# Performance work log

Measured on AMD Instinct MI355X. Metric: run time of the kernel, lower is better.

Reference implementation:

```python
import jax, jax.numpy as jnp
import numpy as np

B, L, H, V = 32768, 24, 64, 64
EPS_NORM = 1e-12  # F.normalize eps
EPS_LN = 1e-5     # LayerNorm eps


def setup_inputs() -> dict:
    key = jax.random.key(0)
    ks = jax.random.split(key, 12)
    s = 1.0 / np.sqrt(H)
    init_val = float(np.log(0.9184 / (1.0 - 0.9184)))
    return {
        "seq": jax.random.randint(ks[0], (B, L), 0, V, dtype=jnp.int32),
        "embed": jax.random.normal(ks[1], (V, H), jnp.float32),
        "w1": jax.random.normal(ks[2], (H, 2 * H), jnp.float32) * s,
        "b1": jnp.zeros((2 * H,), jnp.float32),
        "w2": jax.random.normal(ks[3], (2 * H, H), jnp.float32) * s,
        "b2": jnp.zeros((H,), jnp.float32),
        "ln_g": jnp.ones((H,), jnp.float32),
        "ln_b": jnp.zeros((H,), jnp.float32),
        "rp_w": jax.random.normal(ks[4], (H, H), jnp.float32) * s,
        "rp_b": jnp.zeros((H,), jnp.float32),
        "out_w": jax.random.normal(ks[5], (H, V), jnp.float32) * s,
        "out_b": jnp.zeros((V,), jnp.float32),
        "alpha_logits": jnp.full((L,), init_val, jnp.float32),
    }


def _layernorm(x, g, b):
    mu = jnp.mean(x, axis=-1, keepdims=True)
    var = jnp.mean(jnp.square(x - mu), axis=-1, keepdims=True)
    return (x - mu) * jax.lax.rsqrt(var + EPS_LN) * g + b


def reference(seq, embed, w1, b1, w2, b2, ln_g, ln_b, rp_w, rp_b, out_w, out_b, alpha_logits):
    h = embed[seq]  # [B, L, H]
    ff = jax.nn.relu(h @ w1 + b1) @ w2 + b2
    h = _layernorm(h + ff, ln_g, ln_b)

    alphas = jax.nn.sigmoid(alpha_logits) * 0.49 + 0.5  # [L]
    ht = jnp.swapaxes(h[:, :-1, :], 0, 1)  # [L-1, B, H] time-major

    def step(M, inp):
        k, a = inp  # k: [B, H], a: scalar
        kn = k / jnp.maximum(jnp.linalg.norm(k, axis=-1, keepdims=True), EPS_NORM)
        vp = jnp.einsum('bij,bj->bi', M, kn)
        dv = k - vp
        M = M + (1.0 - a) * (dv[:, :, None] * kn[:, None, :])
        return M, None

    M0 = jnp.zeros((seq.shape[0], h.shape[-1], h.shape[-1]), h.dtype)
    M, _ = jax.lax.scan(step, M0, (ht, alphas[:-1]))

    v = jnp.einsum('bij,bj->bi', M, h[:, -1, :])
    return (v @ rp_w + rp_b) @ out_w + out_b  # [B, V]
```

## Files before the change

### kernel.cpp

```cpp
#include <hip/hip_runtime.h>
#include <hip/hip_bf16.h>
#include <math.h>

#define B_SZ 32768
#define L_SZ 24
#define H_SZ 64
#define V_SZ 64

#define KN_WS 0
#define WK_WS 4096
#define NRM_WS 8192
#define B2_WS 8256
#define CF_WS 8320
#define G_WS  8384
#define WS_F  12480

#define ROW 96
#define G_L   0
#define WK_L  4096
#define NRM_L 10240
#define CB_L  10304
#define TO_L  11840
#define LDS_F 13376

__global__ __launch_bounds__(64) void k_tab(
    const float* __restrict__ embed, const float* __restrict__ w1, const float* __restrict__ b1,
    const float* __restrict__ w2, const float* __restrict__ b2,
    const float* __restrict__ ln_g, const float* __restrict__ ln_b,
    const float* __restrict__ rp_w, const float* __restrict__ rp_b,
    const float* __restrict__ out_w, const float* __restrict__ out_b,
    const float* __restrict__ alpha_logits, float* __restrict__ ws)
{
  const int v = blockIdx.x;
  const int j = threadIdx.x;

  if (v < V_SZ) {
    const float ev = embed[v * H_SZ + j];
    float h0 = b1[j], h1 = b1[j + 64];
    #pragma unroll
    for (int k = 0; k < H_SZ; ++k) {
      const float ek = __shfl(ev, k);
      h0 = fmaf(ek, w1[k * 128 + j], h0);
      h1 = fmaf(ek, w1[k * 128 + 64 + j], h1);
    }
    h0 = fmaxf(h0, 0.0f);
    h1 = fmaxf(h1, 0.0f);
    float x = ev + b2[j];
    #pragma unroll
    for (int k = 0; k < H_SZ; ++k) {
      x = fmaf(__shfl(h0, k), w2[k * H_SZ + j], x);
      x = fmaf(__shfl(h1, k), w2[(k + 64) * H_SZ + j], x);
    }
    float mu = x;
    #pragma unroll
    for (int m = 1; m < 64; m <<= 1) mu += __shfl_xor(mu, m);
    mu *= (1.0f / 64.0f);
    const float dv = x - mu;
    float var = dv * dv;
    #pragma unroll
    for (int m = 1; m < 64; m <<= 1) var += __shfl_xor(var, m);
    var *= (1.0f / 64.0f);
    const float y = dv * rsqrtf(var + 1e-5f) * ln_g[j] + ln_b[j];
    float n2 = y * y;
    #pragma unroll
    for (int m = 1; m < 64; m <<= 1) n2 += __shfl_xor(n2, m);
    const float nrm = sqrtf(n2);
    const float rn = 1.0f / fmaxf(nrm, 1e-12f);
    ws[KN_WS + v * H_SZ + j] = y * rn;
    if (j == 0) ws[NRM_WS + v] = nrm;
    float t1 = 0.0f;
    #pragma unroll
    for (int k = 0; k < H_SZ; ++k) t1 = fmaf(__shfl(y, k), rp_w[k * H_SZ + j], t1);
    float wk = 0.0f;
    #pragma unroll
    for (int k = 0; k < H_SZ; ++k) wk = fmaf(__shfl(t1, k), out_w[k * V_SZ + j], wk);
    ws[WK_WS + v * H_SZ + j] = wk;
  } else {
    float s = out_b[j];
    #pragma unroll
    for (int k = 0; k < H_SZ; ++k) s = fmaf(rp_b[k], out_w[k * V_SZ + j], s);
    ws[B2_WS + j] = s;
    if (j < L_SZ) {
      float cf = 0.0f;
      if (j < L_SZ - 1) {
        const float a = 1.0f / (1.0f + expf(-alpha_logits[j])) * 0.49f + 0.5f;
        cf = 1.0f - a;
      }
      ws[CF_WS + j] = cf;
    }
  }
}

__global__ __launch_bounds__(64) void k_gram(float* __restrict__ ws)
{
  const int u = blockIdx.x;
  const int j = threadIdx.x;
  const float a = ws[KN_WS + u * H_SZ + j];
  float r[64];
  const float4* rp = (const float4*)(ws + KN_WS + j * H_SZ);
  #pragma unroll
  for (int i = 0; i < 16; ++i) {
    const float4 f = rp[i];
    r[4 * i] = f.x; r[4 * i + 1] = f.y; r[4 * i + 2] = f.z; r[4 * i + 3] = f.w;
  }
  float s = 0.0f;
  #pragma unroll
  for (int k = 0; k < 64; ++k) s = fmaf(__shfl(a, k), r[k], s);
  ws[G_WS + u * H_SZ + j] = s;
}

__global__ __launch_bounds__(256) void k_scan(
    const int* __restrict__ seq, const float* __restrict__ ws, float* __restrict__ out)
{
  __shared__ float lds[LDS_F];
  const int tid = threadIdx.x;
  const float4* ws4 = (const float4*)ws;

  for (int i = tid; i < 1024; i += 256)
    ((float4*)(lds + G_L))[i] = ws4[G_WS / 4 + i];
  for (int i = tid; i < 1024; i += 256) {
    const float4 f = ws4[WK_WS / 4 + i];
    const int r = i >> 4;
    const int c = (i & 15) * 4;
    *(float4*)(lds + WK_L + r * ROW + 12 * (c >> 3) + (c & 7)) = f;
  }
  if (tid < 16) ((float4*)(lds + NRM_L))[tid] = ws4[NRM_WS / 4 + tid];
  __syncthreads();

  const int lane = tid & 63;
  const int wv = tid >> 6;
  const float* cfg = ws + CF_WS;

  if (lane < 16) {
    const int ab = wv * 16 + lane;
    const int batch = blockIdx.x * 64 + ab;
    int g[24];
    const int4* sp = (const int4*)(seq + batch * L_SZ);
    #pragma unroll
    for (int i = 0; i < 6; ++i) {
      const int4 t4 = sp[i];
      g[4 * i] = t4.x; g[4 * i + 1] = t4.y; g[4 * i + 2] = t4.z; g[4 * i + 3] = t4.w;
    }
    int* tob = (int*)lds + TO_L + ab * 24;
    #pragma unroll
    for (int i = 0; i < 6; ++i)
      ((int4*)tob)[i] = make_int4(g[4 * i] * ROW, g[4 * i + 1] * ROW,
                                  g[4 * i + 2] * ROW, g[4 * i + 3] * ROW);
    const int q = g[23];
    const float nl = lds[NRM_L + q];
    const float* Gt = lds + G_L;
    float* cb = lds + CB_L + ab * 24;
    float P[23];
    #pragma unroll
    for (int t = 0; t < 23; ++t) P[t] = 0.0f;
    #pragma unroll
    for (int s = 22; s >= 0; --s) {
      const float base = nl * Gt[(g[s] << 6) + q];
      const float cs = cfg[s] * (base - P[s]);
      cb[s] = cs;
      #pragma unroll
      for (int t = 0; t < s; ++t)
        P[t] = fmaf(cs, Gt[(g[t] << 6) + g[s]], P[t]);
    }
    cb[23] = 0.0f;
  }
  __syncthreads();

  const int grp = lane >> 3;
  const int s8 = lane & 7;
  const int cbse = 12 * s8;
  const float* wkL = lds + WK_L;
  const float* b2g = ws + B2_WS + s8 * 8;
  const float4 bA = *(const float4*)(b2g);
  const float4 bB = *(const float4*)(b2g + 4);

  #pragma unroll
  for (int it = 0; it < 2; ++it) {
    const int ab = wv * 16 + it * 8 + grp;
    const int batch = blockIdx.x * 64 + ab;
    float cv[24]; int tv[24];
    const float4* cp = (const float4*)(lds + CB_L + ab * 24);
    const int4* tp = (const int4*)((const int*)lds + TO_L + ab * 24);
    #pragma unroll
    for (int i = 0; i < 6; ++i) {
      const float4 f = cp[i];
      cv[4 * i] = f.x; cv[4 * i + 1] = f.y; cv[4 * i + 2] = f.z; cv[4 * i + 3] = f.w;
      const int4 t4 = tp[i];
      tv[4 * i] = t4.x; tv[4 * i + 1] = t4.y; tv[4 * i + 2] = t4.z; tv[4 * i + 3] = t4.w;
    }
    float oa[8] = {bA.x, bA.y, bA.z, bA.w, bB.x, bB.y, bB.z, bB.w};
    #pragma unroll
    for (int t = 0; t < 23; ++t) {
      const float c = cv[t];
      const float* wr = wkL + tv[t] + cbse;
      const float4 wa = *(const float4*)wr;
      const float4 wb = *(const float4*)(wr + 4);
      oa[0] = fmaf(c, wa.x, oa[0]); oa[1] = fmaf(c, wa.y, oa[1]);
      oa[2] = fmaf(c, wa.z, oa[2]); oa[3] = fmaf(c, wa.w, oa[3]);
      oa[4] = fmaf(c, wb.x, oa[4]); oa[5] = fmaf(c, wb.y, oa[5]);
      oa[6] = fmaf(c, wb.z, oa[6]); oa[7] = fmaf(c, wb.w, oa[7]);
    }
    float4* op = (float4*)(out + batch * V_SZ + s8 * 8);
    op[0] = make_float4(oa[0], oa[1], oa[2], oa[3]);
    op[1] = make_float4(oa[4], oa[5], oa[6], oa[7]);
  }
}

extern "C" void kernel_launch(void* const* d_in, const int* in_sizes, int n_in,
                              void* d_out, int out_size, void* d_ws, size_t ws_size,
                              hipStream_t stream)
{
  const int*   seq          = (const int*)d_in[0];
  const float* embed        = (const float*)d_in[1];
  const float* w1           = (const float*)d_in[2];
  const float* b1           = (const float*)d_in[3];
  const float* w2           = (const float*)d_in[4];
  const float* b2           = (const float*)d_in[5];
  const float* ln_g         = (const float*)d_in[6];
  const float* ln_b         = (const float*)d_in[7];
  const float* rp_w         = (const float*)d_in[8];
  const float* rp_b         = (const float*)d_in[9];
  const float* out_w        = (const float*)d_in[10];
  const float* out_b        = (const float*)d_in[11];
  const float* alpha_logits = (const float*)d_in[12];
  float* ws   = (float*)d_ws;
  float* outp = (float*)d_out;

  hipLaunchKernelGGL(k_tab, dim3(V_SZ + 1), dim3(64), 0, stream,
                     embed, w1, b1, w2, b2, ln_g, ln_b,
                     rp_w, rp_b, out_w, out_b, alpha_logits, ws);
  hipLaunchKernelGGL(k_gram, dim3(V_SZ), dim3(64), 0, stream, ws);
  hipLaunchKernelGGL(k_scan, dim3(B_SZ / 64), dim3(256), 0, stream,
                     seq, ws, outp);
}
```

Before: 27.84 us.

## Shrink scan blocks to one wave so every lane runs a batch recurrence

The scan kernel now uses 64-thread blocks instead of 256-thread blocks. All 64 lanes compute the backward coefficient recurrence, one batch each, where before only 16 lanes per wave did. Token indices are packed four per int in LDS. The norm, bias and coefficient tail is staged in LDS instead of read from global memory. The trade-off is fewer waves per CU: table staging and the output accumulation (now 8 iterations per wave) run on a single wave with less latency hiding.

```diff
diff --git a/kernel.cpp b/kernel.cpp
--- a/kernel.cpp
+++ b/kernel.cpp
@@ -16,12 +16,12 @@
 #define WS_F  12480
 
 #define ROW 96
-#define G_L   0
-#define WK_L  4096
-#define NRM_L 10240
-#define CB_L  10304
-#define TO_L  11840
-#define LDS_F 13376
+#define G_L    0
+#define WK_L   4096
+#define C_L    10240
+#define TK_L   12032
+#define TAIL_L 12544
+#define LDS_F  12704
 
 __global__ __launch_bounds__(64) void k_tab(
     const float* __restrict__ embed, const float* __restrict__ w1, const float* __restrict__ b1,
@@ -109,31 +109,32 @@
   ws[G_WS + u * H_SZ + j] = s;
 }
 
-__global__ __launch_bounds__(256) void k_scan(
+__global__ __launch_bounds__(64) void k_scan(
     const int* __restrict__ seq, const float* __restrict__ ws, float* __restrict__ out)
 {
   __shared__ float lds[LDS_F];
-  const int tid = threadIdx.x;
+  const int lane = threadIdx.x;
   const float4* ws4 = (const float4*)ws;
 
-  for (int i = tid; i < 1024; i += 256)
-    ((float4*)(lds + G_L))[i] = ws4[G_WS / 4 + i];
-  for (int i = tid; i < 1024; i += 256) {
+  float4* g4 = (float4*)(lds + G_L);
+  for (int i = lane; i < 1024; i += 64) g4[i] = ws4[G_WS / 4 + i];
+  for (int i = lane; i < 1024; i += 64) {
     const float4 f = ws4[WK_WS / 4 + i];
     const int r = i >> 4;
-    const int c = (i & 15) * 4;
-    *(float4*)(lds + WK_L + r * ROW + 12 * (c >> 3) + (c & 7)) = f;
-  }
-  if (tid < 16) ((float4*)(lds + NRM_L))[tid] = ws4[NRM_WS / 4 + tid];
+    const int c4 = (i & 15) * 4;
+    *(float4*)(lds + WK_L + r * ROW + 12 * (c4 >> 3) + (c4 & 4)) = f;
+  }
+  if (lane < 38) ((float4*)(lds + TAIL_L))[lane] = ws4[NRM_WS / 4 + lane];
   __syncthreads();
 
-  const int lane = tid & 63;
-  const int wv = tid >> 6;
-  const float* cfg = ws + CF_WS;
-
-  if (lane < 16) {
-    const int ab = wv * 16 + lane;
-    const int batch = blockIdx.x * 64 + ab;
+  const float* nrmL = lds + TAIL_L;
+  const float* b2L  = lds + TAIL_L + 64;
+  const float* cfL  = lds + TAIL_L + 128;
+  const float* Gt   = lds + G_L;
+
+  const int batch0 = blockIdx.x * 64;
+  {
+    const int batch = batch0 + lane;
     int g[24];
     const int4* sp = (const int4*)(seq + batch * L_SZ);
     #pragma unroll
@@ -141,58 +142,71 @@
       const int4 t4 = sp[i];
       g[4 * i] = t4.x; g[4 * i + 1] = t4.y; g[4 * i + 2] = t4.z; g[4 * i + 3] = t4.w;
     }
-    int* tob = (int*)lds + TO_L + ab * 24;
+    int tw[8];
     #pragma unroll
     for (int i = 0; i < 6; ++i)
-      ((int4*)tob)[i] = make_int4(g[4 * i] * ROW, g[4 * i + 1] * ROW,
-                                  g[4 * i + 2] * ROW, g[4 * i + 3] * ROW);
+      tw[i] = g[4 * i] | (g[4 * i + 1] << 8) | (g[4 * i + 2] << 16) | (g[4 * i + 3] << 24);
+    tw[6] = 0; tw[7] = 0;
+    int* tkb = (int*)lds + TK_L + lane * 8;
+    ((int4*)tkb)[0] = make_int4(tw[0], tw[1], tw[2], tw[3]);
+    ((int4*)tkb)[1] = make_int4(tw[4], tw[5], tw[6], tw[7]);
+
+    float cfv[24];
+    #pragma unroll
+    for (int i = 0; i < 6; ++i) {
+      const float4 f = ((const float4*)cfL)[i];
+      cfv[4 * i] = f.x; cfv[4 * i + 1] = f.y; cfv[4 * i + 2] = f.z; cfv[4 * i + 3] = f.w;
+    }
+
     const int q = g[23];
-    const float nl = lds[NRM_L + q];
-    const float* Gt = lds + G_L;
-    float* cb = lds + CB_L + ab * 24;
-    float P[23];
+    const float nl = nrmL[q];
+    float P[23], carr[24];
     #pragma unroll
     for (int t = 0; t < 23; ++t) P[t] = 0.0f;
     #pragma unroll
     for (int s = 22; s >= 0; --s) {
       const float base = nl * Gt[(g[s] << 6) + q];
-      const float cs = cfg[s] * (base - P[s]);
-      cb[s] = cs;
+      const float cs = cfv[s] * (base - P[s]);
+      carr[s] = cs;
       #pragma unroll
       for (int t = 0; t < s; ++t)
         P[t] = fmaf(cs, Gt[(g[t] << 6) + g[s]], P[t]);
     }
-    cb[23] = 0.0f;
+    carr[23] = 0.0f;
+    float* cb = lds + C_L + lane * 28;
+    #pragma unroll
+    for (int i = 0; i < 6; ++i)
+      ((float4*)cb)[i] = make_float4(carr[4 * i], carr[4 * i + 1], carr[4 * i + 2], carr[4 * i + 3]);
   }
   __syncthreads();
 
   const int grp = lane >> 3;
   const int s8 = lane & 7;
-  const int cbse = 12 * s8;
+  const int cb12 = 12 * s8;
+  const float4 bA = ((const float4*)(b2L + s8 * 8))[0];
+  const float4 bB = ((const float4*)(b2L + s8 * 8))[1];
   const float* wkL = lds + WK_L;
-  const float* b2g = ws + B2_WS + s8 * 8;
-  const float4 bA = *(const float4*)(b2g);
-  const float4 bB = *(const float4*)(b2g + 4);
 
   #pragma unroll
-  for (int it = 0; it < 2; ++it) {
-    const int ab = wv * 16 + it * 8 + grp;
-    const int batch = blockIdx.x * 64 + ab;
-    float cv[24]; int tv[24];
-    const float4* cp = (const float4*)(lds + CB_L + ab * 24);
-    const int4* tp = (const int4*)((const int*)lds + TO_L + ab * 24);
+  for (int it = 0; it < 8; ++it) {
+    const int ab = it * 8 + grp;
+    float cv[24];
+    const float4* cp = (const float4*)(lds + C_L + ab * 28);
     #pragma unroll
     for (int i = 0; i < 6; ++i) {
       const float4 f = cp[i];
       cv[4 * i] = f.x; cv[4 * i + 1] = f.y; cv[4 * i + 2] = f.z; cv[4 * i + 3] = f.w;
-      const int4 t4 = tp[i];
-      tv[4 * i] = t4.x; tv[4 * i + 1] = t4.y; tv[4 * i + 2] = t4.z; tv[4 * i + 3] = t4.w;
-    }
+    }
+    const int4* tp = (const int4*)((const int*)lds + TK_L + ab * 8);
+    const int4 ta = tp[0], tb = tp[1];
+    int tw[6] = {ta.x, ta.y, ta.z, ta.w, tb.x, tb.y};
+
     float oa[8] = {bA.x, bA.y, bA.z, bA.w, bB.x, bB.y, bB.z, bB.w};
     #pragma unroll
     for (int t = 0; t < 23; ++t) {
       const float c = cv[t];
-      const float* wr = wkL + tv[t] + cbse;
+      const int tok = (tw[t >> 2] >> ((t & 3) * 8)) & 63;
+      const float* wr = wkL + tok * ROW + cb12;
       const float4 wa = *(const float4*)wr;
       const float4 wb = *(const float4*)(wr + 4);
       oa[0] = fmaf(c, wa.x, oa[0]); oa[1] = fmaf(c, wa.y, oa[1]);
@@ -200,7 +214,7 @@
       oa[4] = fmaf(c, wb.x, oa[4]); oa[5] = fmaf(c, wb.y, oa[5]);
       oa[6] = fmaf(c, wb.z, oa[6]); oa[7] = fmaf(c, wb.w, oa[7]);
     }
-    float4* op = (float4*)(out + batch * V_SZ + s8 * 8);
+    float4* op = (float4*)(out + (batch0 + ab) * V_SZ + s8 * 8);
     op[0] = make_float4(oa[0], oa[1], oa[2], oa[3]);
     op[1] = make_float4(oa[4], oa[5], oa[6], oa[7]);
   }
@@ -230,6 +244,6 @@
                      embed, w1, b1, w2, b2, ln_g, ln_b,
                      rp_w, rp_b, out_w, out_b, alpha_logits, ws);
   hipLaunchKernelGGL(k_gram, dim3(V_SZ), dim3(64), 0, stream, ws);
-  hipLaunchKernelGGL(k_scan, dim3(B_SZ / 64), dim3(256), 0, stream,
+  hipLaunchKernelGGL(k_scan, dim3(B_SZ / 64), dim3(64), 0, stream,
                      seq, ws, outp);
 }
```

After: 34.14 us. 22.6% more time.

## Scatter scan coefficients into dense token histogram and project via split-bf16 MFMA

Applied to the files above, without the earlier changes.

Rather than gathering 23 wk rows per batch and doing fp32 FMAs, each batch's coefficients are scatter-added with LDS atomics into a dense 64-wide weight row over vocabulary tokens. The resulting 64x64 tile per block is multiplied by the transposed wk table using bf16 MFMA, with hi/lo splitting (three products) to keep roughly fp32 accuracy. The k_gw kernel now also precomputes the transposed hi/lo bf16 wk table. This trades gather-heavy LDS traffic for extra LDS staging, atomics, conversions and syncs, plus some precision risk.

```diff
diff --git a/kernel.cpp b/kernel.cpp
--- a/kernel.cpp
+++ b/kernel.cpp
@@ -7,21 +7,30 @@
 #define H_SZ 64
 #define V_SZ 64
 
-#define KN_WS 0
-#define WK_WS 4096
-#define NRM_WS 8192
-#define B2_WS 8256
-#define CF_WS 8320
-#define G_WS  8384
-#define WS_F  12480
-
-#define ROW 96
-#define G_L   0
-#define WK_L  4096
-#define NRM_L 10240
-#define CB_L  10304
-#define TO_L  11840
-#define LDS_F 13376
+#define KN_O    0
+#define WK_O    4096
+#define G_O     8192
+#define WKTH_O  12288
+#define WKTL_O  14592
+#define TAIL_O  16896
+#define WS_DW   17056
+
+#define G_L     0
+#define WKTH_L  4096
+#define WKTL_L  6400
+#define TAIL_L  8704
+#define W32_L   8864
+#define WH_L    12960
+#define WL_L    15264
+#define LDS_DW  17568
+
+typedef __attribute__((ext_vector_type(8))) short short8v;
+typedef __attribute__((ext_vector_type(4))) float f32x4;
+
+static __device__ __forceinline__ unsigned short bf_hi(float x) {
+  const unsigned b = __float_as_uint(x);
+  return (unsigned short)((b + 0x7FFF + ((b >> 16) & 1)) >> 16);
+}
 
 __global__ __launch_bounds__(64) void k_tab(
     const float* __restrict__ embed, const float* __restrict__ w1, const float* __restrict__ b1,
@@ -66,38 +75,38 @@
     for (int m = 1; m < 64; m <<= 1) n2 += __shfl_xor(n2, m);
     const float nrm = sqrtf(n2);
     const float rn = 1.0f / fmaxf(nrm, 1e-12f);
-    ws[KN_WS + v * H_SZ + j] = y * rn;
-    if (j == 0) ws[NRM_WS + v] = nrm;
+    ws[KN_O + v * H_SZ + j] = y * rn;
+    if (j == 0) ws[TAIL_O + v] = nrm;
     float t1 = 0.0f;
     #pragma unroll
     for (int k = 0; k < H_SZ; ++k) t1 = fmaf(__shfl(y, k), rp_w[k * H_SZ + j], t1);
     float wk = 0.0f;
     #pragma unroll
     for (int k = 0; k < H_SZ; ++k) wk = fmaf(__shfl(t1, k), out_w[k * V_SZ + j], wk);
-    ws[WK_WS + v * H_SZ + j] = wk;
+    ws[WK_O + v * H_SZ + j] = wk;
   } else {
     float s = out_b[j];
     #pragma unroll
     for (int k = 0; k < H_SZ; ++k) s = fmaf(rp_b[k], out_w[k * V_SZ + j], s);
-    ws[B2_WS + j] = s;
-    if (j < L_SZ) {
+    ws[TAIL_O + 64 + j] = s;
+    if (j < 32) {
       float cf = 0.0f;
       if (j < L_SZ - 1) {
         const float a = 1.0f / (1.0f + expf(-alpha_logits[j])) * 0.49f + 0.5f;
         cf = 1.0f - a;
       }
-      ws[CF_WS + j] = cf;
-    }
-  }
-}
-
-__global__ __launch_bounds__(64) void k_gram(float* __restrict__ ws)
+      ws[TAIL_O + 128 + j] = cf;
+    }
+  }
+}
+
+__global__ __launch_bounds__(64) void k_gw(float* __restrict__ ws)
 {
   const int u = blockIdx.x;
   const int j = threadIdx.x;
-  const float a = ws[KN_WS + u * H_SZ + j];
+  const float a = ws[KN_O + u * H_SZ + j];
   float r[64];
-  const float4* rp = (const float4*)(ws + KN_WS + j * H_SZ);
+  const float4* rp = (const float4*)(ws + KN_O + j * H_SZ);
   #pragma unroll
   for (int i = 0; i < 16; ++i) {
     const float4 f = rp[i];
@@ -106,103 +115,121 @@
   float s = 0.0f;
   #pragma unroll
   for (int k = 0; k < 64; ++k) s = fmaf(__shfl(a, k), r[k], s);
-  ws[G_WS + u * H_SZ + j] = s;
+  ws[G_O + u * H_SZ + j] = s;
+
+  const float x = ws[WK_O + j * H_SZ + u];
+  const unsigned short hi = bf_hi(x);
+  const float fhi = __uint_as_float((unsigned)hi << 16);
+  const unsigned short lo = bf_hi(x - fhi);
+  unsigned short* wsu = (unsigned short*)ws;
+  wsu[WKTH_O * 2 + u * 72 + j] = hi;
+  wsu[WKTL_O * 2 + u * 72 + j] = lo;
 }
 
 __global__ __launch_bounds__(256) void k_scan(
     const int* __restrict__ seq, const float* __restrict__ ws, float* __restrict__ out)
 {
-  __shared__ float lds[LDS_F];
+  __shared__ float lds[LDS_DW];
   const int tid = threadIdx.x;
   const float4* ws4 = (const float4*)ws;
-
-  for (int i = tid; i < 1024; i += 256)
-    ((float4*)(lds + G_L))[i] = ws4[G_WS / 4 + i];
-  for (int i = tid; i < 1024; i += 256) {
-    const float4 f = ws4[WK_WS / 4 + i];
-    const int r = i >> 4;
-    const int c = (i & 15) * 4;
-    *(float4*)(lds + WK_L + r * ROW + 12 * (c >> 3) + (c & 7)) = f;
-  }
-  if (tid < 16) ((float4*)(lds + NRM_L))[tid] = ws4[NRM_WS / 4 + tid];
+  float4* l4 = (float4*)lds;
+  for (int i = tid; i < (WS_DW - 8192) / 4; i += 256) l4[i] = ws4[2048 + i];
+  const float4 z4 = {0.f, 0.f, 0.f, 0.f};
+  for (int i = tid; i < 1024; i += 256) ((float4*)(lds + W32_L))[i] = z4;
   __syncthreads();
 
   const int lane = tid & 63;
   const int wv = tid >> 6;
-  const float* cfg = ws + CF_WS;
+  const int batch0 = blockIdx.x * 64;
+  const float* Gt = lds + G_L;
 
   if (lane < 16) {
     const int ab = wv * 16 + lane;
-    const int batch = blockIdx.x * 64 + ab;
     int g[24];
-    const int4* sp = (const int4*)(seq + batch * L_SZ);
+    const int4* sp = (const int4*)(seq + (batch0 + ab) * L_SZ);
     #pragma unroll
     for (int i = 0; i < 6; ++i) {
       const int4 t4 = sp[i];
       g[4 * i] = t4.x; g[4 * i + 1] = t4.y; g[4 * i + 2] = t4.z; g[4 * i + 3] = t4.w;
     }
-    int* tob = (int*)lds + TO_L + ab * 24;
-    #pragma unroll
-    for (int i = 0; i < 6; ++i)
-      ((int4*)tob)[i] = make_int4(g[4 * i] * ROW, g[4 * i + 1] * ROW,
-                                  g[4 * i + 2] * ROW, g[4 * i + 3] * ROW);
     const int q = g[23];
-    const float nl = lds[NRM_L + q];
-    const float* Gt = lds + G_L;
-    float* cb = lds + CB_L + ab * 24;
-    float P[23];
+    const float nl = lds[TAIL_L + q];
+    float cfv[24];
+    #pragma unroll
+    for (int i = 0; i < 6; ++i) {
+      const float4 f = ((const float4*)(lds + TAIL_L + 128))[i];
+      cfv[4 * i] = f.x; cfv[4 * i + 1] = f.y; cfv[4 * i + 2] = f.z; cfv[4 * i + 3] = f.w;
+    }
+    float P[23], carr[23];
     #pragma unroll
     for (int t = 0; t < 23; ++t) P[t] = 0.0f;
     #pragma unroll
     for (int s = 22; s >= 0; --s) {
       const float base = nl * Gt[(g[s] << 6) + q];
-      const float cs = cfg[s] * (base - P[s]);
-      cb[s] = cs;
+      const float cs = cfv[s] * (base - P[s]);
+      carr[s] = cs;
       #pragma unroll
       for (int t = 0; t < s; ++t)
         P[t] = fmaf(cs, Gt[(g[t] << 6) + g[s]], P[t]);
     }
-    cb[23] = 0.0f;
+    float* wrow = lds + W32_L + ab * 64;
+    #pragma unroll
+    for (int t = 0; t < 23; ++t)
+      atomicAdd(&wrow[g[t]], carr[t]);
   }
   __syncthreads();
 
-  const int grp = lane >> 3;
-  const int s8 = lane & 7;
-  const int cbse = 12 * s8;
-  const float* wkL = lds + WK_L;
-  const float* b2g = ws + B2_WS + s8 * 8;
-  const float4 bA = *(const float4*)(b2g);
-  const float4 bB = *(const float4*)(b2g + 4);
+  {
+    const int c4 = (lane & 15) * 4;
+    unsigned short* whp = (unsigned short*)(lds + WH_L);
+    unsigned short* wlp = (unsigned short*)(lds + WL_L);
+    #pragma unroll
+    for (int i = 0; i < 4; ++i) {
+      const int row = wv * 16 + (lane >> 4) + i * 4;
+      const float4 f = *(const float4*)(lds + W32_L + row * 64 + c4);
+      ushort4 h, l2;
+      h.x = bf_hi(f.x); h.y = bf_hi(f.y); h.z = bf_hi(f.z); h.w = bf_hi(f.w);
+      l2.x = bf_hi(f.x - __uint_as_float((unsigned)h.x << 16));
+      l2.y = bf_hi(f.y - __uint_as_float((unsigned)h.y << 16));
+      l2.z = bf_hi(f.z - __uint_as_float((unsigned)h.z << 16));
+      l2.w = bf_hi(f.w - __uint_as_float((unsigned)h.w << 16));
+      *(ushort4*)(whp + row * 72 + c4) = h;
+      *(ushort4*)(wlp + row * 72 + c4) = l2;
+    }
+  }
+  __syncthreads();
+
+  const int cl = lane & 15;
+  const int q4 = lane >> 4;
+  const unsigned short* whp = (const unsigned short*)(lds + WH_L);
+  const unsigned short* wlp = (const unsigned short*)(lds + WL_L);
+  const unsigned short* bhp = (const unsigned short*)(lds + WKTH_L);
+  const unsigned short* blp = (const unsigned short*)(lds + WKTL_L);
+
+  const int arow = wv * 16 + cl;
+  const short8v ah0 = *(const short8v*)(whp + arow * 72 + q4 * 8);
+  const short8v ah1 = *(const short8v*)(whp + arow * 72 + 32 + q4 * 8);
+  const short8v al0 = *(const short8v*)(wlp + arow * 72 + q4 * 8);
+  const short8v al1 = *(const short8v*)(wlp + arow * 72 + 32 + q4 * 8);
 
   #pragma unroll
-  for (int it = 0; it < 2; ++it) {
-    const int ab = wv * 16 + it * 8 + grp;
-    const int batch = blockIdx.x * 64 + ab;
-    float cv[24]; int tv[24];
-    const float4* cp = (const float4*)(lds + CB_L + ab * 24);
-    const int4* tp = (const int4*)((const int*)lds + TO_L + ab * 24);
-    #pragma unroll
-    for (int i = 0; i < 6; ++i) {
-      const float4 f = cp[i];
-      cv[4 * i] = f.x; cv[4 * i + 1] = f.y; cv[4 * i + 2] = f.z; cv[4 * i + 3] = f.w;
-      const int4 t4 = tp[i];
-      tv[4 * i] = t4.x; tv[4 * i + 1] = t4.y; tv[4 * i + 2] = t4.z; tv[4 * i + 3] = t4.w;
-    }
-    float oa[8] = {bA.x, bA.y, bA.z, bA.w, bB.x, bB.y, bB.z, bB.w};
-    #pragma unroll
-    for (int t = 0; t < 23; ++t) {
-      const float c = cv[t];
-      const float* wr = wkL + tv[t] + cbse;
-      const float4 wa = *(const float4*)wr;
-      const float4 wb = *(const float4*)(wr + 4);
-      oa[0] = fmaf(c, wa.x, oa[0]); oa[1] = fmaf(c, wa.y, oa[1]);
-      oa[2] = fmaf(c, wa.z, oa[2]); oa[3] = fmaf(c, wa.w, oa[3]);
-      oa[4] = fmaf(c, wb.x, oa[4]); oa[5] = fmaf(c, wb.y, oa[5]);
-      oa[6] = fmaf(c, wb.z, oa[6]); oa[7] = fmaf(c, wb.w, oa[7]);
-    }
-    float4* op = (float4*)(out + batch * V_SZ + s8 * 8);
-    op[0] = make_float4(oa[0], oa[1], oa[2], oa[3]);
-    op[1] = make_float4(oa[4], oa[5], oa[6], oa[7]);
+  for (int ct = 0; ct < 4; ++ct) {
+    const int col = ct * 16 + cl;
+    const short8v bh0 = *(const short8v*)(bhp + col * 72 + q4 * 8);
+    const short8v bh1 = *(const short8v*)(bhp + col * 72 + 32 + q4 * 8);
+    const short8v bl0 = *(const short8v*)(blp + col * 72 + q4 * 8);
+    const short8v bl1 = *(const short8v*)(blp + col * 72 + 32 + q4 * 8);
+    const float b2v = lds[TAIL_L + 64 + col];
+    f32x4 acc = {b2v, b2v, b2v, b2v};
+    acc = __builtin_amdgcn_mfma_f32_16x16x32_bf16(ah0, bh0, acc, 0, 0, 0);
+    acc = __builtin_amdgcn_mfma_f32_16x16x32_bf16(ah1, bh1, acc, 0, 0, 0);
+    acc = __builtin_amdgcn_mfma_f32_16x16x32_bf16(al0, bh0, acc, 0, 0, 0);
+    acc = __builtin_amdgcn_mfma_f32_16x16x32_bf16(al1, bh1, acc, 0, 0, 0);
+    acc = __builtin_amdgcn_mfma_f32_16x16x32_bf16(ah0, bl0, acc, 0, 0, 0);
+    acc = __builtin_amdgcn_mfma_f32_16x16x32_bf16(ah1, bl1, acc, 0, 0, 0);
+    #pragma unroll
+    for (int rr = 0; rr < 4; ++rr)
+      out[(batch0 + wv * 16 + q4 * 4 + rr) * V_SZ + col] = acc[rr];
   }
 }
 
@@ -229,7 +256,7 @@
   hipLaunchKernelGGL(k_tab, dim3(V_SZ + 1), dim3(64), 0, stream,
                      embed, w1, b1, w2, b2, ln_g, ln_b,
                      rp_w, rp_b, out_w, out_b, alpha_logits, ws);
-  hipLaunchKernelGGL(k_gram, dim3(V_SZ), dim3(64), 0, stream, ws);
+  hipLaunchKernelGGL(k_gw, dim3(V_SZ), dim3(64), 0, stream, ws);
   hipLaunchKernelGGL(k_scan, dim3(B_SZ / 64), dim3(256), 0, stream,
                      seq, ws, outp);
 }
```

Result: slower. 29.86 us (+7.2%).
